# Optimization experiments

Hardware: AMD Instinct MI355X
Metric: run time of the kernel (lower is better)

The kernel has to match this reference:

```python
import jax, jax.numpy as jnp
import numpy as np

N_NODES = 100000
N_EDGES = 800000


def setup_inputs() -> dict:
    key = jax.random.key(0)
    ks = jax.random.split(key, 9)
    def glorot(k, shape):
        lim = float(np.sqrt(6.0 / (shape[0] + shape[1])))
        return jax.random.uniform(k, shape, jnp.float32, -lim, lim)
    return {
        "x": jax.random.normal(ks[0], (N_NODES, 4), jnp.float32),
        "edge_index": jax.random.randint(ks[1], (2, N_EDGES), 0, N_NODES, jnp.int64),
        "edge_weight": jax.random.uniform(ks[2], (N_EDGES,), jnp.float32),
        "W1": glorot(ks[3], (4, 128)),
        "b1": jnp.zeros((128,), jnp.float32),
        "W2": glorot(ks[4], (128, 64)),
        "b2": jnp.zeros((64,), jnp.float32),
        "W3": glorot(ks[5], (64, 1)),
        "b3": jnp.zeros((1,), jnp.float32),
    }


def reference(x, edge_index, edge_weight, W1, b1, W2, b2, W3, b3):
    N = x.shape[0]
    # PyG GCNConv: add self loops (weight 1) and symmetric normalization.
    loop = jnp.arange(N)
    src = jnp.concatenate([edge_index[0], loop])  # [E+N]
    dst = jnp.concatenate([edge_index[1], loop])  # [E+N]
    w = jnp.concatenate([edge_weight, jnp.ones((N,), x.dtype)])
    deg = jax.ops.segment_sum(w, dst, num_segments=N)  # weighted in-degree
    dis = jnp.where(deg > 0, jax.lax.rsqrt(jnp.maximum(deg, 1e-12)), 0.0)
    norm = dis[src] * w * dis[dst]  # [E+N]

    def conv(h, W, b):
        h = h @ W                      # [N, F_out] transform first (F_out small)
        msg = norm[:, None] * h[src]   # gather + scale per edge
        return jax.ops.segment_sum(msg, dst, num_segments=N) + b

    h = jax.nn.relu(conv(x, W1, b1))
    h = jax.nn.relu(conv(h, W2, b2))
    return conv(h, W3, b3)
```

## Files before the change

kernel.cpp:

```cpp
#include <hip/hip_runtime.h>
#include <hip/hip_fp16.h>


constexpr int N = 100000;
constexpr int E = 800000;
constexpr int NBKT = 391;
constexpr int BCAP = 3072;
constexpr int GC = 125;
constexpr int CHUNK = 6400;

static inline int cdiv(int a, int b) { return (a + b - 1) / b; }

typedef __attribute__((ext_vector_type(8))) _Float16 f16x8;
typedef __attribute__((ext_vector_type(4))) float f32x4;

__global__ void k_zero(int* __restrict__ bucket_cursor) {
    int i = blockIdx.x * blockDim.x + threadIdx.x;
    if (i < NBKT) bucket_cursor[i] = 0;
}

__global__ __launch_bounds__(256) void k_coarse(const int* __restrict__ src,
                                                const int* __restrict__ dst,
                                                const float* __restrict__ w,
                                                int* __restrict__ bucket_cursor,
                                                int2* __restrict__ sorted) {
    __shared__ int hist[NBKT];
    __shared__ int base[NBKT];
    int t = threadIdx.x;
    for (int i = t; i < NBKT; i += 256) hist[i] = 0;
    __syncthreads();
    int begin = blockIdx.x * CHUNK;
    int ranks[25];
#pragma unroll
    for (int i = 0; i < 25; i++) {
        int e = begin + i * 256 + t;
        ranks[i] = atomicAdd(&hist[dst[e] >> 8], 1);
    }
    __syncthreads();
    for (int i = t; i < NBKT; i += 256) {
        int h = hist[i];
        base[i] = h ? atomicAdd(&bucket_cursor[i], h) : 0;
    }
    __syncthreads();
#pragma unroll
    for (int i = 0; i < 25; i++) {
        int e = begin + i * 256 + t;
        int d = dst[e], b = d >> 8;
        int pos = base[b] + ranks[i];
        if (pos < BCAP)
            sorted[(size_t)b * BCAP + pos] =
                make_int2(src[e] | ((d & 255) << 17), __float_as_int(w[e]));
    }
}

__global__ __launch_bounds__(256) void k_fine(const int2* __restrict__ sorted,
                                              const int* __restrict__ bucket_cursor,
                                              int cap, int2* __restrict__ payload,
                                              int* __restrict__ cursor,
                                              float* __restrict__ dis) {
    __shared__ int   ncnt[256];
    __shared__ float nwsum[256];
    int t = threadIdx.x, b = blockIdx.x;
    ncnt[t] = 1;
    nwsum[t] = 1.0f;
    __syncthreads();
    int cnt = bucket_cursor[b]; if (cnt > BCAP) cnt = BCAP;
    const int2* seg = sorted + (size_t)b * BCAP;
    for (int i = t; i < cnt; i += 256) {
        int2 r = seg[i];
        int s = r.x & 0x1FFFF, dlo = r.x >> 17;
        int pos = atomicAdd(&ncnt[dlo], 1);
        atomicAdd(&nwsum[dlo], __int_as_float(r.y));
        if (pos < cap)
            payload[(size_t)(b * 256 + dlo) * cap + pos] = make_int2(s, r.y);
    }
    __syncthreads();
    int n = b * 256 + t;
    if (n < N) {
        int c = ncnt[t]; if (c > cap) c = cap;
        int2* row = payload + (size_t)n * cap;
        row[0] = make_int2(n, __float_as_int(1.0f));
        int cpad = (c + 7) & ~7;
        for (int e = c; e < cpad; e++) row[e] = make_int2(0, 0);
        cursor[n] = c;
        dis[n] = rsqrtf(nwsum[t]);
    }
}

__global__ __launch_bounds__(256) void k_agg1(const float* __restrict__ x,
                                              const float* __restrict__ dis,
                                              const int* __restrict__ cursor,
                                              int2* __restrict__ payload, int cap,
                                              float* __restrict__ agg1) {
    int t = threadIdx.x, lane = t & 63, wave = t >> 6;
    int nsub = lane >> 4, slot = (lane >> 2) & 3, feat = lane & 3;
    int n = (blockIdx.x * 4 + wave) * 4 + nsub;
    float di = dis[n];
    int cnt = cursor[n];
    int2* row = payload + (size_t)n * cap;
    int iters = (cnt + 3) >> 2;
    float acc = 0.f;
    for (int it = 0; it < iters; it++) {
        int e = it * 4 + slot;
        int2 p = row[e];
        float nm = dis[p.x] * __int_as_float(p.y) * di;
        float xv = x[p.x * 4 + feat];
        acc = fmaf(nm, xv, acc);
        if (feat == 0) row[e].y = __float_as_int(nm);
    }
    acc += __shfl_xor(acc, 4);
    acc += __shfl_xor(acc, 8);
    if (slot == 0) agg1[n * 4 + feat] = acc;
}

constexpr int HROW = 136;
__global__ __launch_bounds__(256) void k_fused_l1(const float4* __restrict__ agg1,
                                                  const float* __restrict__ W1,
                                                  const float* __restrict__ b1,
                                                  const float* __restrict__ W2,
                                                  __half* __restrict__ y2h) {
    __shared__ _Float16 h1lds[4][16 * HROW];
    int t = threadIdx.x, wave = t >> 6, lane = t & 63;
    int q = lane >> 4, c = lane & 15;
    _Float16* sh = h1lds[wave];

    int k1 = lane, k2 = lane + 64;
    float w10 = W1[0 * 128 + k1], w11 = W1[1 * 128 + k1];
    float w12 = W1[2 * 128 + k1], w13 = W1[3 * 128 + k1], bb1 = b1[k1];
    float w20 = W1[0 * 128 + k2], w21 = W1[1 * 128 + k2];
    float w22 = W1[2 * 128 + k2], w23 = W1[3 * 128 + k2], bb2 = b1[k2];

    f16x8 Bf[4][4];
#pragma unroll
    for (int kt = 0; kt < 4; kt++)
#pragma unroll
        for (int nt = 0; nt < 4; nt++)
#pragma unroll
            for (int j = 0; j < 8; j++)
                Bf[kt][nt][j] = (_Float16)W2[(kt * 32 + q * 8 + j) * 64 + nt * 16 + c];

    int wave_id = blockIdx.x * 4 + wave;
#pragma unroll
    for (int g = 0; g < 2; g++) {
        int n0 = (wave_id * 2 + g) * 16;
        if (n0 >= N) break;
#pragma unroll
        for (int m = 0; m < 16; m++) {
            float4 a = agg1[n0 + m];
            float v1 = bb1, v2 = bb2;
            v1 = fmaf(a.x, w10, v1); v1 = fmaf(a.y, w11, v1);
            v1 = fmaf(a.z, w12, v1); v1 = fmaf(a.w, w13, v1);
            v2 = fmaf(a.x, w20, v2); v2 = fmaf(a.y, w21, v2);
            v2 = fmaf(a.z, w22, v2); v2 = fmaf(a.w, w23, v2);
            sh[m * HROW + k1] = (_Float16)fmaxf(v1, 0.f);
            sh[m * HROW + k2] = (_Float16)fmaxf(v2, 0.f);
        }
        f32x4 C[4] = {{0.f, 0.f, 0.f, 0.f}, {0.f, 0.f, 0.f, 0.f},
                      {0.f, 0.f, 0.f, 0.f}, {0.f, 0.f, 0.f, 0.f}};
#pragma unroll
        for (int kt = 0; kt < 4; kt++) {
            f16x8 A = *(const f16x8*)&sh[c * HROW + kt * 32 + q * 8];
#pragma unroll
            for (int nt = 0; nt < 4; nt++)
                C[nt] = __builtin_amdgcn_mfma_f32_16x16x32_f16(A, Bf[kt][nt], C[nt], 0, 0, 0);
        }
#pragma unroll
        for (int nt = 0; nt < 4; nt++)
#pragma unroll
            for (int r = 0; r < 4; r++) {
                int node = n0 + q * 4 + r;
                y2h[(size_t)node * 64 + nt * 16 + c] = __float2half(C[nt][r]);
            }
    }
}

__global__ __launch_bounds__(256) void k_agg2(const __half* __restrict__ y2h,
                                              const int* __restrict__ cursor,
                                              const int2* __restrict__ payload, int cap,
                                              const float* __restrict__ b2,
                                              const float* __restrict__ W3,
                                              float* __restrict__ s_out) {
    int t = threadIdx.x, lane = t & 63, wave = t >> 6;
    int nsub = lane >> 4, slot = (lane >> 3) & 1, k = lane & 7;
    int n = (blockIdx.x * 4 + wave) * 4 + nsub;
    float b2v[8], w3v[8];
#pragma unroll
    for (int j = 0; j < 8; j++) { b2v[j] = b2[k * 8 + j]; w3v[j] = W3[k * 8 + j]; }
    int cnt = cursor[n];
    const int2* row = payload + (size_t)n * cap;
    int iters = (cnt + 1) >> 1;
    float acc[8] = {0.f, 0.f, 0.f, 0.f, 0.f, 0.f, 0.f, 0.f};
    for (int it = 0; it < iters; it++) {
        int2 p = row[it * 2 + slot];
        float nm = __int_as_float(p.y);
        f16x8 v = *(const f16x8*)(y2h + (size_t)p.x * 64 + k * 8);
#pragma unroll
        for (int j = 0; j < 8; j++)
            acc[j] = fmaf(nm, (float)v[j], acc[j]);
    }
#pragma unroll
    for (int j = 0; j < 8; j++) acc[j] += __shfl_xor(acc[j], 8);
    float p_ = 0.f;
#pragma unroll
    for (int j = 0; j < 8; j++) {
        float h = fmaxf(acc[j] + b2v[j], 0.f);
        p_ = fmaf(h, w3v[j], p_);
    }
    p_ += __shfl_xor(p_, 1);
    p_ += __shfl_xor(p_, 2);
    p_ += __shfl_xor(p_, 4);
    if (slot == 0 && k == 0) s_out[n] = p_;
}

__global__ __launch_bounds__(256) void k_agg3(const float* __restrict__ s,
                                              const int* __restrict__ cursor,
                                              const int2* __restrict__ payload, int cap,
                                              const float* __restrict__ b3,
                                              float* __restrict__ out) {
    int t = threadIdx.x, lane = t & 63, wave = t >> 6;
    int nsub = lane >> 3, slot = lane & 7;
    int n = (blockIdx.x * 4 + wave) * 8 + nsub;
    int cnt = cursor[n];
    const int2* row = payload + (size_t)n * cap;
    int iters = (cnt + 7) >> 3;
    float acc = 0.f;
    for (int it = 0; it < iters; it++) {
        int2 p = row[it * 8 + slot];
        acc = fmaf(__int_as_float(p.y), s[p.x], acc);
    }
    acc += __shfl_xor(acc, 1);
    acc += __shfl_xor(acc, 2);
    acc += __shfl_xor(acc, 4);
    if (slot == 0) out[n] = acc + b3[0];
}

extern "C" void kernel_launch(void* const* d_in, const int* in_sizes, int n_in,
                              void* d_out, int out_size, void* d_ws, size_t ws_size,
                              hipStream_t stream) {
    const float* x  = (const float*)d_in[0];
    const int*   ei = (const int*)d_in[1];
    const int* src = ei;
    const int* dst = ei + E;
    const float* w  = (const float*)d_in[2];
    const float* W1 = (const float*)d_in[3];
    const float* b1 = (const float*)d_in[4];
    const float* W2 = (const float*)d_in[5];
    const float* b2 = (const float*)d_in[6];
    const float* W3 = (const float*)d_in[7];
    const float* b3 = (const float*)d_in[8];
    float* out = (float*)d_out;

    int*    bcur    = (int*)d_ws;
    int*    cursor  = bcur + 512;
    float*  dis     = (float*)(cursor + N);
    float*  agg1    = dis + N;
    __half* y2h     = (__half*)(agg1 + 4 * N);
    float*  s       = agg1;
    int2*   sorted  = (int2*)((char*)y2h + (size_t)64 * N * sizeof(__half));
    int2*   payload = sorted + (size_t)NBKT * BCAP;
    size_t fixed_bytes = (size_t)(512 + 2 * N + 4 * N) * 4 + (size_t)64 * N * 2
                       + (size_t)NBKT * BCAP * 8;
    int cap = (int)((ws_size - fixed_bytes) / ((size_t)N * 8));
    if (cap > 64) cap = 64;

    k_zero    <<<cdiv(NBKT, 256), 256, 0, stream>>>(bcur);
    k_coarse  <<<GC,              256, 0, stream>>>(src, dst, w, bcur, sorted);
    k_fine    <<<NBKT,            256, 0, stream>>>(sorted, bcur, cap, payload, cursor, dis);
    k_agg1    <<<N / 16,          256, 0, stream>>>(x, dis, cursor, payload, cap, agg1);
    k_fused_l1<<<cdiv(N / 16, 8), 256, 0, stream>>>((const float4*)agg1, W1, b1, W2, y2h);
    k_agg2    <<<N / 16,          256, 0, stream>>>(y2h, cursor, payload, cap, b2, W3, s);
    k_agg3    <<<N / 32,          256, 0, stream>>>(s, cursor, payload, cap, b3, out);
}
```

Before: 169.9 us.

## Stage coarse bucket scatter in LDS and widen fine-sort blocks

The coarse binning kernel now gathers each chunk's records in shared memory, grouped by bucket through a block-level prefix scan. It then writes each bucket's run to global memory contiguously, replacing the scattered per-edge stores. The fine kernel runs 512 threads per block, so each bucket's records are processed with twice the parallelism. The cost is about 50KB of LDS per coarse block, an extra scan with several barriers, and a serial per-bucket copy loop in each thread.

```diff
diff --git a/kernel.cpp b/kernel.cpp
--- a/kernel.cpp
+++ b/kernel.cpp
@@ -24,36 +24,60 @@
                                                 const float* __restrict__ w,
                                                 int* __restrict__ bucket_cursor,
                                                 int2* __restrict__ sorted) {
-    __shared__ int hist[NBKT];
-    __shared__ int base[NBKT];
+    __shared__ int  hist[NBKT];
+    __shared__ int  lofs[512];
+    __shared__ int  gbase[NBKT];
+    __shared__ int2 recs[CHUNK];
     int t = threadIdx.x;
     for (int i = t; i < NBKT; i += 256) hist[i] = 0;
     __syncthreads();
     int begin = blockIdx.x * CHUNK;
-    int ranks[25];
+    int packed[25];
+#pragma unroll
+    for (int i = 0; i < 25; i++) {
+        int d = dst[begin + i * 256 + t];
+        int b = d >> 8;
+        int rank = atomicAdd(&hist[b], 1);
+        packed[i] = (rank << 17) | (b << 8) | (d & 255);
+    }
+    __syncthreads();
+    int v0 = hist[t];
+    int v1 = (256 + t < NBKT) ? hist[256 + t] : 0;
+    lofs[t] = v0; lofs[256 + t] = v1;
+    __syncthreads();
+    for (int off = 1; off < 256; off <<= 1) {
+        int u0 = (t >= off) ? lofs[t - off] : 0;
+        int u1 = (t >= off) ? lofs[256 + t - off] : 0;
+        __syncthreads();
+        lofs[t] += u0; lofs[256 + t] += u1;
+        __syncthreads();
+    }
+    int tot0 = lofs[255];
+    lofs[t] -= v0;
+    lofs[256 + t] += tot0 - v1;
+    __syncthreads();
+    for (int i = t; i < NBKT; i += 256) {
+        int h = hist[i];
+        gbase[i] = h ? atomicAdd(&bucket_cursor[i], h) : 0;
+    }
+    __syncthreads();
 #pragma unroll
     for (int i = 0; i < 25; i++) {
         int e = begin + i * 256 + t;
-        ranks[i] = atomicAdd(&hist[dst[e] >> 8], 1);
-    }
-    __syncthreads();
-    for (int i = t; i < NBKT; i += 256) {
-        int h = hist[i];
-        base[i] = h ? atomicAdd(&bucket_cursor[i], h) : 0;
-    }
-    __syncthreads();
-#pragma unroll
-    for (int i = 0; i < 25; i++) {
-        int e = begin + i * 256 + t;
-        int d = dst[e], b = d >> 8;
-        int pos = base[b] + ranks[i];
-        if (pos < BCAP)
-            sorted[(size_t)b * BCAP + pos] =
-                make_int2(src[e] | ((d & 255) << 17), __float_as_int(w[e]));
-    }
-}
-
-__global__ __launch_bounds__(256) void k_fine(const int2* __restrict__ sorted,
+        int pk = packed[i];
+        int b = (pk >> 8) & 511, rank = pk >> 17, dlo = pk & 255;
+        recs[lofs[b] + rank] = make_int2(src[e] | (dlo << 17), __float_as_int(w[e]));
+    }
+    __syncthreads();
+    for (int b = t; b < NBKT; b += 256) {
+        int cnt = hist[b], lo = lofs[b], gb = gbase[b];
+        int lim = BCAP - gb; if (cnt > lim) cnt = lim;
+        int2* dstp = sorted + (size_t)b * BCAP + gb;
+        for (int j = 0; j < cnt; j++) dstp[j] = recs[lo + j];
+    }
+}
+
+__global__ __launch_bounds__(512) void k_fine(const int2* __restrict__ sorted,
                                               const int* __restrict__ bucket_cursor,
                                               int cap, int2* __restrict__ payload,
                                               int* __restrict__ cursor,
@@ -61,12 +85,11 @@
     __shared__ int   ncnt[256];
     __shared__ float nwsum[256];
     int t = threadIdx.x, b = blockIdx.x;
-    ncnt[t] = 1;
-    nwsum[t] = 1.0f;
+    if (t < 256) { ncnt[t] = 1; nwsum[t] = 1.0f; }
     __syncthreads();
     int cnt = bucket_cursor[b]; if (cnt > BCAP) cnt = BCAP;
     const int2* seg = sorted + (size_t)b * BCAP;
-    for (int i = t; i < cnt; i += 256) {
+    for (int i = t; i < cnt; i += 512) {
         int2 r = seg[i];
         int s = r.x & 0x1FFFF, dlo = r.x >> 17;
         int pos = atomicAdd(&ncnt[dlo], 1);
@@ -76,7 +99,7 @@
     }
     __syncthreads();
     int n = b * 256 + t;
-    if (n < N) {
+    if (t < 256 && n < N) {
         int c = ncnt[t]; if (c > cap) c = cap;
         int2* row = payload + (size_t)n * cap;
         row[0] = make_int2(n, __float_as_int(1.0f));
@@ -265,7 +288,7 @@
 
     k_zero    <<<cdiv(NBKT, 256), 256, 0, stream>>>(bcur);
     k_coarse  <<<GC,              256, 0, stream>>>(src, dst, w, bcur, sorted);
-    k_fine    <<<NBKT,            256, 0, stream>>>(sorted, bcur, cap, payload, cursor, dis);
+    k_fine    <<<NBKT,            512, 0, stream>>>(sorted, bcur, cap, payload, cursor, dis);
     k_agg1    <<<N / 16,          256, 0, stream>>>(x, dis, cursor, payload, cap, agg1);
     k_fused_l1<<<cdiv(N / 16, 8), 256, 0, stream>>>((const float4*)agg1, W1, b1, W2, y2h);
     k_agg2    <<<N / 16,          256, 0, stream>>>(y2h, cursor, payload, cap, b2, W3, s);
```

After: 163.7 us. 3.6% less time.
